# Performance work log

Measured on AMD Instinct MI355X. Metric: run time of the kernel, lower is better.

## Reference

```python
import jax, jax.numpy as jnp
import numpy as np

N_NODES = 100000
N_EDGES = 3200000
N_GRAPHS = 64
F_IN = 64
NUM_CLASSES = 10
CHROM = 21


def _glorot(key, shape):
    fan_in, fan_out = shape
    lim = (6.0 / (fan_in + fan_out)) ** 0.5
    return jax.random.uniform(key, shape, jnp.float32, -lim, lim)


def setup_inputs() -> dict:
    key = jax.random.key(0)
    ks = jax.random.split(key, 16)
    x = jax.random.normal(ks[0], (N_NODES, F_IN), jnp.float32)
    edge_index = jax.random.randint(ks[1], (2, N_EDGES), 0, N_NODES, jnp.int32)
    batch = jnp.sort(jax.random.randint(ks[2], (N_NODES,), 0, N_GRAPHS, jnp.int32))
    return {
        "x": x,
        "edge_index": edge_index,
        "batch": batch,
        # SAGEConv1: 64 -> 16
        "W1l": _glorot(ks[3], (F_IN, 16)), "b1": jnp.zeros((16,), jnp.float32),
        "W1r": _glorot(ks[4], (F_IN, 16)),
        # SAGEConv2: 16 -> 32
        "W2l": _glorot(ks[5], (16, 32)), "b2": jnp.zeros((32,), jnp.float32),
        "W2r": _glorot(ks[6], (16, 32)),
        # SAGEConv3: 32 -> 21
        "W3l": _glorot(ks[7], (32, CHROM)), "b3": jnp.zeros((CHROM,), jnp.float32),
        "W3r": _glorot(ks[8], (32, CHROM)),
        # classifier: 32 -> num_classes
        "Wc": _glorot(ks[9], (32, NUM_CLASSES)), "bc": jnp.zeros((NUM_CLASSES,), jnp.float32),
    }


def _sage_conv(x, src, dst, Wl, b, Wr):
    # mean aggregation of source features at target nodes (PyG SAGEConv default)
    agg = jax.ops.segment_sum(x[src], dst, num_segments=N_NODES)
    cnt = jax.ops.segment_sum(jnp.ones((src.shape[0],), x.dtype), dst, num_segments=N_NODES)
    mean = agg / jnp.maximum(cnt, 1.0)[:, None]
    return mean @ Wl + b + x @ Wr


def reference(x, edge_index, batch, W1l, b1, W1r, W2l, b2, W2r, W3l, b3, W3r, Wc, bc):
    src, dst = edge_index[0], edge_index[1]
    h = jax.nn.relu(_sage_conv(x, src, dst, W1l, b1, W1r))
    h2 = _sage_conv(h, src, dst, W2l, b2, W2r)          # pooled pre-relu
    color = _sage_conv(jax.nn.relu(h2), src, dst, W3l, b3, W3r)
    # global_mean_pool over graphs
    gsum = jax.ops.segment_sum(h2, batch, num_segments=N_GRAPHS)
    gcnt = jax.ops.segment_sum(jnp.ones((h2.shape[0],), h2.dtype), batch, num_segments=N_GRAPHS)
    pooled = gsum / jnp.maximum(gcnt, 1.0)[:, None]
    # dropout p=0.3 is identity in eval mode
    classif = pooled @ Wc + bc
    return classif, color
```

## Files before the change

kernel.cpp:

```cpp
#include <hip/hip_runtime.h>
#include <hip/hip_fp16.h>
#include <cstdint>
#include <cstddef>

#define N_NODES  100000
#define N_EDGES  3200000
#define N_GRAPHS 64

#define BQBITS   9
#define BQ       512
#define NBUCK    196
#define TILE     4096
#define NBLK     782
#define POOL_SLICES 8
#define PADB     4608


__global__ void kp1_hist(const int* __restrict__ dst, int* __restrict__ gh, int ne) {
    __shared__ int h[NBUCK];
    for (int i = threadIdx.x; i < NBUCK; i += 256) h[i] = 0;
    __syncthreads();
    int base = blockIdx.x * TILE;
    for (int i = threadIdx.x; i < TILE; i += 256) {
        int e = base + i;
        if (e < ne) atomicAdd(&h[dst[e] >> BQBITS], 1);
    }
    __syncthreads();
    for (int i = threadIdx.x; i < NBUCK; i += 256) gh[i * NBLK + blockIdx.x] = h[i];
}

__global__ void kp1_scanA(int* __restrict__ gh, int* __restrict__ btotal) {
    int q = blockIdx.x;
    __shared__ int ts[256];
    int v[4];
    int tsum = 0;
#pragma unroll
    for (int u = 0; u < 4; ++u) {
        int idx = threadIdx.x * 4 + u;
        v[u] = (idx < NBLK) ? gh[q * NBLK + idx] : 0;
        tsum += v[u];
    }
    ts[threadIdx.x] = tsum;
    __syncthreads();
    for (int off = 1; off < 256; off <<= 1) {
        int t = (threadIdx.x >= off) ? ts[threadIdx.x - off] : 0;
        __syncthreads();
        ts[threadIdx.x] += t;
        __syncthreads();
    }
    int run = ts[threadIdx.x] - tsum;
#pragma unroll
    for (int u = 0; u < 4; ++u) {
        int idx = threadIdx.x * 4 + u;
        if (idx < NBLK) gh[q * NBLK + idx] = run;
        run += v[u];
    }
    if (threadIdx.x == 255) btotal[q] = ts[255];
}

__global__ void kp1_scanB(const int* __restrict__ btotal, int* __restrict__ bstart) {
    __shared__ int s[256];
    int v = (threadIdx.x < NBUCK) ? btotal[threadIdx.x] : 0;
    s[threadIdx.x] = v;
    __syncthreads();
    for (int off = 1; off < 256; off <<= 1) {
        int t = (threadIdx.x >= off) ? s[threadIdx.x - off] : 0;
        __syncthreads();
        s[threadIdx.x] += t;
        __syncthreads();
    }
    if (threadIdx.x < NBUCK) bstart[threadIdx.x] = s[threadIdx.x] - v;
    if (threadIdx.x == 0) bstart[NBUCK] = N_EDGES;
}

__global__ __launch_bounds__(256) void kp1_scatter(
        const int* __restrict__ src, const int* __restrict__ dst,
        const int* __restrict__ gh, const int* __restrict__ bstart,
        unsigned* __restrict__ tmp, int ne) {
    __shared__ unsigned sed[TILE];
    __shared__ int lcnt[NBUCK];
    __shared__ int lofs[NBUCK + 1];
    __shared__ int fill[NBUCK];
    __shared__ int delta[NBUCK];
    __shared__ int ts[256];
    for (int i = threadIdx.x; i < NBUCK; i += 256) { lcnt[i] = 0; fill[i] = 0; }
    __syncthreads();
    int base = blockIdx.x * TILE;
    int nh = ne - base; if (nh > TILE) nh = TILE;
    int myq[16]; unsigned myw[16];
#pragma unroll
    for (int u = 0; u < 16; ++u) {
        int i = u * 256 + threadIdx.x;
        myq[u] = -1;
        if (i < nh) {
            int d = dst[base + i], s = src[base + i];
            int q = d >> BQBITS;
            myq[u] = q;
            myw[u] = ((unsigned)(d & (BQ - 1)) << 17) | (unsigned)s;
            atomicAdd(&lcnt[q], 1);
        }
    }
    __syncthreads();
    int v = (threadIdx.x < NBUCK) ? lcnt[threadIdx.x] : 0;
    ts[threadIdx.x] = v;
    __syncthreads();
    for (int off = 1; off < 256; off <<= 1) {
        int t = (threadIdx.x >= off) ? ts[threadIdx.x - off] : 0;
        __syncthreads();
        ts[threadIdx.x] += t;
        __syncthreads();
    }
    if (threadIdx.x < NBUCK) {
        int start = ts[threadIdx.x] - v;
        lofs[threadIdx.x] = start;
        delta[threadIdx.x] = bstart[threadIdx.x] + gh[threadIdx.x * NBLK + blockIdx.x] - start;
    }
    if (threadIdx.x == NBUCK - 1) lofs[NBUCK] = ts[threadIdx.x];
    __syncthreads();
#pragma unroll
    for (int u = 0; u < 16; ++u) {
        if (myq[u] >= 0) {
            int r = atomicAdd(&fill[myq[u]], 1);
            sed[lofs[myq[u]] + r] = myw[u];
        }
    }
    __syncthreads();
    for (int p = threadIdx.x; p < nh; p += 256) {
        int lo = 0, hi = NBUCK;
        while (hi - lo > 1) { int mid = (lo + hi) >> 1; if (lofs[mid] <= p) lo = mid; else hi = mid; }
        tmp[p + delta[lo]] = sed[p];
    }
}

__global__ void kp2(const unsigned* __restrict__ tmp, const int* __restrict__ bstart,
                    int* __restrict__ rs, int* __restrict__ deg, int* __restrict__ perm) {
    int q = blockIdx.x;
    int beg = bstart[q], end = bstart[q + 1];
    int m = end - beg;
    int pbase = ((beg + 7) & ~7) + q * PADB;
    __shared__ int cnt[BQ];
    __shared__ int lofs[BQ];
    __shared__ int fill[BQ];
    if (threadIdx.x < BQ) { cnt[threadIdx.x] = 0; fill[threadIdx.x] = 0; }
    __syncthreads();
    for (int p = threadIdx.x; p < m; p += 1024)
        atomicAdd(&cnt[tmp[beg + p] >> 17], 1);
    __syncthreads();
    int pc = 0;
    if (threadIdx.x < BQ) { pc = (cnt[threadIdx.x] + 7) & ~7; lofs[threadIdx.x] = pc; }
    __syncthreads();
    for (int off = 1; off < BQ; off <<= 1) {
        int t = 0;
        if (threadIdx.x < BQ && threadIdx.x >= off) t = lofs[threadIdx.x - off];
        __syncthreads();
        if (threadIdx.x < BQ) lofs[threadIdx.x] += t;
        __syncthreads();
    }
    if (threadIdx.x < BQ) {
        int node = q * BQ + threadIdx.x;
        if (node < N_NODES) {
            int st = lofs[threadIdx.x] - pc;
            rs[node] = pbase + st;
            deg[node] = cnt[threadIdx.x];
            for (int i = cnt[threadIdx.x]; i < pc; ++i)
                perm[pbase + st + i] = N_NODES;
        }
    }
    __syncthreads();
    for (int p = threadIdx.x; p < m; p += 1024) {
        unsigned w = tmp[beg + p];
        int dl = w >> 17;
        int s = w & 0x1FFFF;
        int r = atomicAdd(&fill[dl], 1);
        int st = lofs[dl] - ((cnt[dl] + 7) & ~7);
        perm[pbase + st + r] = s;
    }
}


__global__ void k_zero(__half* __restrict__ y1z, __half* __restrict__ hz,
                       __half* __restrict__ y3z, float* __restrict__ gsum) {
    int t = threadIdx.x;
    if (t < 16) { y1z[t] = __half(0.f); hz[t] = __half(0.f); }
    if (t < 24) y3z[t] = __half(0.f);
    for (int i = t; i < N_GRAPHS * 32; i += 256) gsum[i] = 0.f;
}


__global__ void k_t1(const float* __restrict__ x, const float* __restrict__ W1l,
                     const float* __restrict__ W1r, const float* __restrict__ b1,
                     __half* __restrict__ y1, float* __restrict__ s1, int n) {
    __shared__ float wl[64 * 16], wr[64 * 16], bb[16];
    for (int i = threadIdx.x; i < 64 * 16; i += blockDim.x) { wl[i] = W1l[i]; wr[i] = W1r[i]; }
    if (threadIdx.x < 16) bb[threadIdx.x] = b1[threadIdx.x];
    __syncthreads();
    int node = blockIdx.x * blockDim.x + threadIdx.x;
    if (node >= n) return;
    const float4* xr = reinterpret_cast<const float4*>(x + (size_t)node * 64);
    float accl[16], accr[16];
#pragma unroll
    for (int j = 0; j < 16; ++j) { accl[j] = 0.f; accr[j] = 0.f; }
#pragma unroll
    for (int q = 0; q < 16; ++q) {
        float4 v = xr[q];
        float xs[4] = {v.x, v.y, v.z, v.w};
#pragma unroll
        for (int u = 0; u < 4; ++u) {
            int k = q * 4 + u;
            float xv = xs[u];
#pragma unroll
            for (int j = 0; j < 16; ++j) {
                accl[j] += xv * wl[k * 16 + j];
                accr[j] += xv * wr[k * 16 + j];
            }
        }
    }
    alignas(16) __half yh[16];
#pragma unroll
    for (int j = 0; j < 16; ++j) yh[j] = __float2half(accl[j]);
    uint4* y4 = reinterpret_cast<uint4*>(y1 + (size_t)node * 16);
    const uint4* yv = reinterpret_cast<const uint4*>(yh);
    y4[0] = yv[0]; y4[1] = yv[1];
    float4* s4 = reinterpret_cast<float4*>(s1 + (size_t)node * 16);
#pragma unroll
    for (int q = 0; q < 4; ++q)
        s4[q] = make_float4(accr[q*4+0] + bb[q*4+0], accr[q*4+1] + bb[q*4+1],
                            accr[q*4+2] + bb[q*4+2], accr[q*4+3] + bb[q*4+3]);
}

__global__ void k_t2(const float* __restrict__ mean2, const __half* __restrict__ h,
                     const float* __restrict__ W2l, const float* __restrict__ W2r,
                     const float* __restrict__ b2, float* __restrict__ h2, int n) {
    __shared__ float wl[16 * 32], wr[16 * 32], bb[32];
    for (int i = threadIdx.x; i < 16 * 32; i += blockDim.x) { wl[i] = W2l[i]; wr[i] = W2r[i]; }
    if (threadIdx.x < 32) bb[threadIdx.x] = b2[threadIdx.x];
    __syncthreads();
    int node = blockIdx.x * blockDim.x + threadIdx.x;
    if (node >= n) return;
    float m[16], hh[16];
    const float4* m4 = reinterpret_cast<const float4*>(mean2 + (size_t)node * 16);
#pragma unroll
    for (int q = 0; q < 4; ++q) {
        float4 a = m4[q];
        m[q*4+0]=a.x; m[q*4+1]=a.y; m[q*4+2]=a.z; m[q*4+3]=a.w;
    }
    alignas(16) __half hv[16];
    const uint4* hp = reinterpret_cast<const uint4*>(h + (size_t)node * 16);
    uint4* hvp = reinterpret_cast<uint4*>(hv);
    hvp[0] = hp[0]; hvp[1] = hp[1];
#pragma unroll
    for (int k = 0; k < 16; ++k) hh[k] = __half2float(hv[k]);
    float acc[32];
#pragma unroll
    for (int j = 0; j < 32; ++j) acc[j] = bb[j];
#pragma unroll
    for (int k = 0; k < 16; ++k) {
#pragma unroll
        for (int j = 0; j < 32; ++j)
            acc[j] += m[k] * wl[k * 32 + j] + hh[k] * wr[k * 32 + j];
    }
    float4* o4 = reinterpret_cast<float4*>(h2 + (size_t)node * 32);
#pragma unroll
    for (int q = 0; q < 8; ++q)
        o4[q] = make_float4(acc[q*4+0], acc[q*4+1], acc[q*4+2], acc[q*4+3]);
}

__global__ void k_t3(const float* __restrict__ h2, const float* __restrict__ W3l,
                     const float* __restrict__ W3r, const float* __restrict__ b3,
                     __half* __restrict__ y3, float* __restrict__ s3, int n) {
    __shared__ float wl[32 * 21], wr[32 * 21], bb[21];
    for (int i = threadIdx.x; i < 32 * 21; i += blockDim.x) { wl[i] = W3l[i]; wr[i] = W3r[i]; }
    if (threadIdx.x < 21) bb[threadIdx.x] = b3[threadIdx.x];
    __syncthreads();
    int node = blockIdx.x * blockDim.x + threadIdx.x;
    if (node >= n) return;
    float z[32];
    const float4* h4 = reinterpret_cast<const float4*>(h2 + (size_t)node * 32);
#pragma unroll
    for (int q = 0; q < 8; ++q) {
        float4 v = h4[q];
        z[q*4+0] = fmaxf(v.x, 0.f); z[q*4+1] = fmaxf(v.y, 0.f);
        z[q*4+2] = fmaxf(v.z, 0.f); z[q*4+3] = fmaxf(v.w, 0.f);
    }
    float a[21], c[21];
#pragma unroll
    for (int j = 0; j < 21; ++j) { a[j] = 0.f; c[j] = bb[j]; }
#pragma unroll
    for (int k = 0; k < 32; ++k) {
#pragma unroll
        for (int j = 0; j < 21; ++j) {
            a[j] += z[k] * wl[k * 21 + j];
            c[j] += z[k] * wr[k * 21 + j];
        }
    }
    alignas(16) __half yh[24];
#pragma unroll
    for (int j = 0; j < 21; ++j) yh[j] = __float2half(a[j]);
    yh[21] = __half(0.f); yh[22] = __half(0.f); yh[23] = __half(0.f);
    uint4* yp = reinterpret_cast<uint4*>(y3 + (size_t)node * 24);
    const uint4* yv = reinterpret_cast<const uint4*>(yh);
    yp[0] = yv[0]; yp[1] = yv[1]; yp[2] = yv[2];
    float* so = s3 + (size_t)node * 24;
#pragma unroll
    for (int j = 0; j < 21; ++j) so[j] = c[j];
    so[21] = 0.f; so[22] = 0.f; so[23] = 0.f;
}


__device__ __forceinline__ void acc8(uint4 v, float* a) {
    __half2 h0 = *reinterpret_cast<__half2*>(&v.x);
    __half2 h1 = *reinterpret_cast<__half2*>(&v.y);
    __half2 h2 = *reinterpret_cast<__half2*>(&v.z);
    __half2 h3 = *reinterpret_cast<__half2*>(&v.w);
    float2 f0 = __half22float2(h0), f1 = __half22float2(h1);
    float2 f2 = __half22float2(h2), f3 = __half22float2(h3);
    a[0] += f0.x; a[1] += f0.y; a[2] += f1.x; a[3] += f1.y;
    a[4] += f2.x; a[5] += f2.y; a[6] += f3.x; a[7] += f3.y;
}

template <bool RELU, bool SELF, bool OUT_HALF>
__global__ void k_agg16(const uint4* __restrict__ y, const int* __restrict__ rs,
                        const int* __restrict__ deg, const int* __restrict__ perm,
                        const float* __restrict__ self, void* __restrict__ outp,
                        int n_nodes) {
    int t = blockIdx.x * blockDim.x + threadIdx.x;
    int node = t >> 1;
    int f = t & 1;
    if (node >= n_nodes) return;
    int beg = rs[node];
    int d = deg[node];
    int pend = beg + ((d + 7) & ~7);
    float a[8];
#pragma unroll
    for (int j = 0; j < 8; ++j) a[j] = 0.f;
    for (int e = beg; e < pend; e += 8) {
        const int4* pp = reinterpret_cast<const int4*>(perm + e);
        int4 p0 = pp[0];
        int4 p1 = pp[1];
        uint4 v0 = y[(size_t)p0.x * 2 + f];
        uint4 v1 = y[(size_t)p0.y * 2 + f];
        uint4 v2 = y[(size_t)p0.z * 2 + f];
        uint4 v3 = y[(size_t)p0.w * 2 + f];
        uint4 v4 = y[(size_t)p1.x * 2 + f];
        uint4 v5 = y[(size_t)p1.y * 2 + f];
        uint4 v6 = y[(size_t)p1.z * 2 + f];
        uint4 v7 = y[(size_t)p1.w * 2 + f];
        acc8(v0, a); acc8(v1, a); acc8(v2, a); acc8(v3, a);
        acc8(v4, a); acc8(v5, a); acc8(v6, a); acc8(v7, a);
    }
    float inv = 1.0f / fmaxf((float)d, 1.0f);
#pragma unroll
    for (int j = 0; j < 8; ++j) a[j] *= inv;
    if (SELF) {
        const float4* sp = reinterpret_cast<const float4*>(self + (size_t)node * 16 + f * 8);
        float4 s0 = sp[0], s1 = sp[1];
        a[0] += s0.x; a[1] += s0.y; a[2] += s0.z; a[3] += s0.w;
        a[4] += s1.x; a[5] += s1.y; a[6] += s1.z; a[7] += s1.w;
    }
    if (RELU) {
#pragma unroll
        for (int j = 0; j < 8; ++j) a[j] = fmaxf(a[j], 0.f);
    }
    if constexpr (OUT_HALF) {
        __half2 p0 = __floats2half2_rn(a[0], a[1]);
        __half2 p1 = __floats2half2_rn(a[2], a[3]);
        __half2 p2 = __floats2half2_rn(a[4], a[5]);
        __half2 p3 = __floats2half2_rn(a[6], a[7]);
        uint4 o;
        o.x = *reinterpret_cast<unsigned*>(&p0);
        o.y = *reinterpret_cast<unsigned*>(&p1);
        o.z = *reinterpret_cast<unsigned*>(&p2);
        o.w = *reinterpret_cast<unsigned*>(&p3);
        ((uint4*)outp)[(size_t)node * 2 + f] = o;
    } else {
        float4* op = (float4*)outp + (size_t)node * 4 + f * 2;
        op[0] = make_float4(a[0], a[1], a[2], a[3]);
        op[1] = make_float4(a[4], a[5], a[6], a[7]);
    }
}

__global__ void k_agg21(const uint4* __restrict__ y, const int* __restrict__ rs,
                        const int* __restrict__ deg, const int* __restrict__ perm,
                        const float* __restrict__ self24, float* __restrict__ outp,
                        int n_nodes) {
    int t = blockIdx.x * blockDim.x + threadIdx.x;
    int node = t / 3;
    int f = t - node * 3;
    if (node >= n_nodes) return;
    int beg = rs[node];
    int d = deg[node];
    int pend = beg + ((d + 7) & ~7);
    float a[8];
#pragma unroll
    for (int j = 0; j < 8; ++j) a[j] = 0.f;
    for (int e = beg; e < pend; e += 8) {
        const int4* pp = reinterpret_cast<const int4*>(perm + e);
        int4 p0 = pp[0];
        int4 p1 = pp[1];
        uint4 v0 = y[(size_t)p0.x * 3 + f];
        uint4 v1 = y[(size_t)p0.y * 3 + f];
        uint4 v2 = y[(size_t)p0.z * 3 + f];
        uint4 v3 = y[(size_t)p0.w * 3 + f];
        uint4 v4 = y[(size_t)p1.x * 3 + f];
        uint4 v5 = y[(size_t)p1.y * 3 + f];
        uint4 v6 = y[(size_t)p1.z * 3 + f];
        uint4 v7 = y[(size_t)p1.w * 3 + f];
        acc8(v0, a); acc8(v1, a); acc8(v2, a); acc8(v3, a);
        acc8(v4, a); acc8(v5, a); acc8(v6, a); acc8(v7, a);
    }
    float inv = 1.0f / fmaxf((float)d, 1.0f);
    int c0 = f * 8;
    const float4* sp = reinterpret_cast<const float4*>(self24 + (size_t)node * 24 + c0);
    float4 s0 = sp[0], s1 = sp[1];
    float r[8];
    r[0] = a[0] * inv + s0.x; r[1] = a[1] * inv + s0.y;
    r[2] = a[2] * inv + s0.z; r[3] = a[3] * inv + s0.w;
    r[4] = a[4] * inv + s1.x; r[5] = a[5] * inv + s1.y;
    r[6] = a[6] * inv + s1.z; r[7] = a[7] * inv + s1.w;
    float* op = outp + (size_t)node * 21;
    int nlim = 21 - c0;
#pragma unroll
    for (int j = 0; j < 8; ++j)
        if (j < nlim) op[c0 + j] = r[j];
}


__device__ __forceinline__ int lowerb(const int* a, int n, int key) {
    int lo = 0, hi = n;
    while (lo < hi) { int mid = (lo + hi) >> 1; if (a[mid] < key) lo = mid + 1; else hi = mid; }
    return lo;
}

__global__ void k_pool(const float* __restrict__ h2, const int* __restrict__ batch,
                       float* __restrict__ gsum, float* __restrict__ gcnt, int n) {
    int g = blockIdx.x / POOL_SLICES;
    int slice = blockIdx.x - g * POOL_SLICES;
    __shared__ int sbeg, send;
    if (threadIdx.x == 0) { sbeg = lowerb(batch, n, g); send = lowerb(batch, n, g + 1); }
    __syncthreads();
    int beg = sbeg, end = send;
    int f = threadIdx.x & 31;
    int r = threadIdx.x >> 5;
    float acc = 0.f;
    for (int i = beg + slice * 8 + r; i < end; i += POOL_SLICES * 8)
        acc += h2[(size_t)i * 32 + f];
    __shared__ float red[256];
    red[threadIdx.x] = acc;
    __syncthreads();
    if (r == 0) {
        float s = 0.f;
#pragma unroll
        for (int q = 0; q < 8; ++q) s += red[q * 32 + f];
        atomicAdd(&gsum[g * 32 + f], s);
    }
    if (slice == 0 && threadIdx.x == 0) gcnt[g] = (float)(end - beg);
}

__global__ void k_cls(const float* __restrict__ gsum, const float* __restrict__ gcnt,
                      const float* __restrict__ Wc, const float* __restrict__ bc,
                      float* __restrict__ outp) {
    int t = threadIdx.x;
    if (t >= N_GRAPHS * 10) return;
    int g = t / 10, c = t - g * 10;
    float cv = fmaxf(gcnt[g], 1.f);
    float acc = bc[c];
#pragma unroll
    for (int k = 0; k < 32; ++k) acc += (gsum[g * 32 + k] / cv) * Wc[k * 10 + c];
    outp[g * 10 + c] = acc;
}


extern "C" void kernel_launch(void* const* d_in, const int* in_sizes, int n_in,
                              void* d_out, int out_size, void* d_ws, size_t ws_size,
                              hipStream_t stream) {
    const float* x    = (const float*)d_in[0];
    const int*   ei   = (const int*)d_in[1];
    const int*   batch= (const int*)d_in[2];
    const float* W1l  = (const float*)d_in[3];
    const float* b1   = (const float*)d_in[4];
    const float* W1r  = (const float*)d_in[5];
    const float* W2l  = (const float*)d_in[6];
    const float* b2   = (const float*)d_in[7];
    const float* W2r  = (const float*)d_in[8];
    const float* W3l  = (const float*)d_in[9];
    const float* b3   = (const float*)d_in[10];
    const float* W3r  = (const float*)d_in[11];
    const float* Wc   = (const float*)d_in[12];
    const float* bc   = (const float*)d_in[13];
    float* out = (float*)d_out;

    char* ws = (char*)d_ws;
    size_t off = 0;
    auto alloc = [&](size_t bytes) { size_t o = off; off += (bytes + 255) & ~(size_t)255; return o; };

    int*    rs    = (int*)(ws + alloc((size_t)N_NODES * 4));
    int*    deg   = (int*)(ws + alloc((size_t)N_NODES * 4));
    int*    perm  = (int*)(ws + alloc((size_t)(N_EDGES + (size_t)NBUCK * PADB + 64) * 4));
    int*    gh    = (int*)(ws + alloc((size_t)NBUCK * NBLK * 4));
    int*    btotal= (int*)(ws + alloc(256 * 4));
    int*    bstart= (int*)(ws + alloc(260 * 4));
    __half* y1    = (__half*)(ws + alloc((size_t)(N_NODES + 1) * 16 * 2));
    float*  s1    = (float*)(ws + alloc((size_t)N_NODES * 16 * 4));
    __half* h     = (__half*)(ws + alloc((size_t)(N_NODES + 1) * 16 * 2));
    float*  mean2 = (float*)(ws + alloc((size_t)N_NODES * 16 * 4));
    float*  h2    = (float*)(ws + alloc((size_t)N_NODES * 32 * 4));
    __half* y3    = (__half*)(ws + alloc((size_t)(N_NODES + 1) * 24 * 2));
    float*  s3    = (float*)(ws + alloc((size_t)N_NODES * 24 * 4));
    float*  gsum  = (float*)(ws + alloc((size_t)N_GRAPHS * 32 * 4));
    float*  gcnt  = (float*)(ws + alloc((size_t)N_GRAPHS * 4));

    unsigned* tmp = (unsigned*)h2;

    const int* src = ei;
    const int* dst = ei + N_EDGES;

    int nb  = (N_NODES + 255) / 256;
    int g2  = (N_NODES * 2 + 255) / 256;
    int g3  = (N_NODES * 3 + 255) / 256;

    k_zero<<<1, 256, 0, stream>>>(y1 + (size_t)N_NODES * 16, h + (size_t)N_NODES * 16,
                                  y3 + (size_t)N_NODES * 24, gsum);

    kp1_hist   <<<NBLK, 256, 0, stream>>>(dst, gh, N_EDGES);
    kp1_scanA  <<<NBUCK, 256, 0, stream>>>(gh, btotal);
    kp1_scanB  <<<1, 256, 0, stream>>>(btotal, bstart);
    kp1_scatter<<<NBLK, 256, 0, stream>>>(src, dst, gh, bstart, tmp, N_EDGES);
    kp2        <<<NBUCK, 1024, 0, stream>>>(tmp, bstart, rs, deg, perm);

    k_t1<<<nb, 256, 0, stream>>>(x, W1l, W1r, b1, y1, s1, N_NODES);
    k_agg16<true, true, true><<<g2, 256, 0, stream>>>(
        (const uint4*)y1, rs, deg, perm, s1, h, N_NODES);

    k_agg16<false, false, false><<<g2, 256, 0, stream>>>(
        (const uint4*)h, rs, deg, perm, nullptr, mean2, N_NODES);
    k_t2<<<nb, 256, 0, stream>>>(mean2, h, W2l, W2r, b2, h2, N_NODES);

    k_t3<<<nb, 256, 0, stream>>>(h2, W3l, W3r, b3, y3, s3, N_NODES);
    k_agg21<<<g3, 256, 0, stream>>>(
        (const uint4*)y3, rs, deg, perm, s3, out + N_GRAPHS * 10, N_NODES);

    k_pool<<<N_GRAPHS * POOL_SLICES, 256, 0, stream>>>(h2, batch, gsum, gcnt, N_NODES);
    k_cls<<<1, 640, 0, stream>>>(gsum, gcnt, Wc, bc, out);
}
```

Before: 237.8 us.

## Store gathered node features in FP8 e4m3 to halve gather traffic

```diff
diff --git a/kernel.cpp b/kernel.cpp
--- a/kernel.cpp
+++ b/kernel.cpp
@@ -1,5 +1,6 @@
 #include <hip/hip_runtime.h>
 #include <hip/hip_fp16.h>
+#include <hip/hip_fp8.h>
 #include <cstdint>
 #include <cstddef>
 
@@ -178,18 +179,41 @@
 }
 
 
-__global__ void k_zero(__half* __restrict__ y1z, __half* __restrict__ hz,
-                       __half* __restrict__ y3z, float* __restrict__ gsum) {
+__device__ __forceinline__ void accq(uint2 v, float* a) {
+    unsigned x = v.x, y = v.y;
+#pragma unroll
+    for (int j = 0; j < 4; ++j) {
+        __hip_fp8_e4m3 q0, q1;
+        q0.__x = (__hip_fp8_storage_t)((x >> (8 * j)) & 0xFF);
+        q1.__x = (__hip_fp8_storage_t)((y >> (8 * j)) & 0xFF);
+        a[j]     += (float)q0;
+        a[4 + j] += (float)q1;
+    }
+}
+
+__device__ __forceinline__ uint2 pack8_fp8(const float* a) {
+    unsigned lo = 0, hi = 0;
+#pragma unroll
+    for (int j = 0; j < 4; ++j) {
+        lo |= (unsigned)__hip_fp8_e4m3(a[j]).__x << (8 * j);
+        hi |= (unsigned)__hip_fp8_e4m3(a[4 + j]).__x << (8 * j);
+    }
+    uint2 o; o.x = lo; o.y = hi; return o;
+}
+
+
+__global__ void k_zero(uint2* __restrict__ y1qz, uint2* __restrict__ hqz,
+                       unsigned char* __restrict__ y3qz, float* __restrict__ gsum) {
     int t = threadIdx.x;
-    if (t < 16) { y1z[t] = __half(0.f); hz[t] = __half(0.f); }
-    if (t < 24) y3z[t] = __half(0.f);
+    if (t < 2) { y1qz[t] = make_uint2(0, 0); hqz[t] = make_uint2(0, 0); }
+    if (t < 24) y3qz[t] = 0;
     for (int i = t; i < N_GRAPHS * 32; i += 256) gsum[i] = 0.f;
 }
 
 
 __global__ void k_t1(const float* __restrict__ x, const float* __restrict__ W1l,
                      const float* __restrict__ W1r, const float* __restrict__ b1,
-                     __half* __restrict__ y1, float* __restrict__ s1, int n) {
+                     uint2* __restrict__ y1q, float* __restrict__ s1, int n) {
     __shared__ float wl[64 * 16], wr[64 * 16], bb[16];
     for (int i = threadIdx.x; i < 64 * 16; i += blockDim.x) { wl[i] = W1l[i]; wr[i] = W1r[i]; }
     if (threadIdx.x < 16) bb[threadIdx.x] = b1[threadIdx.x];
@@ -215,12 +239,8 @@
             }
         }
     }
-    alignas(16) __half yh[16];
-#pragma unroll
-    for (int j = 0; j < 16; ++j) yh[j] = __float2half(accl[j]);
-    uint4* y4 = reinterpret_cast<uint4*>(y1 + (size_t)node * 16);
-    const uint4* yv = reinterpret_cast<const uint4*>(yh);
-    y4[0] = yv[0]; y4[1] = yv[1];
+    y1q[(size_t)node * 2 + 0] = pack8_fp8(accl);
+    y1q[(size_t)node * 2 + 1] = pack8_fp8(accl + 8);
     float4* s4 = reinterpret_cast<float4*>(s1 + (size_t)node * 16);
 #pragma unroll
     for (int q = 0; q < 4; ++q)
@@ -267,7 +287,7 @@
 
 __global__ void k_t3(const float* __restrict__ h2, const float* __restrict__ W3l,
                      const float* __restrict__ W3r, const float* __restrict__ b3,
-                     __half* __restrict__ y3, float* __restrict__ s3, int n) {
+                     unsigned char* __restrict__ y3q, float* __restrict__ s3, int n) {
     __shared__ float wl[32 * 21], wr[32 * 21], bb[21];
     for (int i = threadIdx.x; i < 32 * 21; i += blockDim.x) { wl[i] = W3l[i]; wr[i] = W3r[i]; }
     if (threadIdx.x < 21) bb[threadIdx.x] = b3[threadIdx.x];
@@ -282,9 +302,10 @@
         z[q*4+0] = fmaxf(v.x, 0.f); z[q*4+1] = fmaxf(v.y, 0.f);
         z[q*4+2] = fmaxf(v.z, 0.f); z[q*4+3] = fmaxf(v.w, 0.f);
     }
-    float a[21], c[21];
+    float a[24], c[21];
 #pragma unroll
     for (int j = 0; j < 21; ++j) { a[j] = 0.f; c[j] = bb[j]; }
+    a[21] = 0.f; a[22] = 0.f; a[23] = 0.f;
 #pragma unroll
     for (int k = 0; k < 32; ++k) {
 #pragma unroll
@@ -293,13 +314,10 @@
             c[j] += z[k] * wr[k * 21 + j];
         }
     }
-    alignas(16) __half yh[24];
-#pragma unroll
-    for (int j = 0; j < 21; ++j) yh[j] = __float2half(a[j]);
-    yh[21] = __half(0.f); yh[22] = __half(0.f); yh[23] = __half(0.f);
-    uint4* yp = reinterpret_cast<uint4*>(y3 + (size_t)node * 24);
-    const uint4* yv = reinterpret_cast<const uint4*>(yh);
-    yp[0] = yv[0]; yp[1] = yv[1]; yp[2] = yv[2];
+    uint2* yp = reinterpret_cast<uint2*>(y3q + (size_t)node * 24);
+    yp[0] = pack8_fp8(a);
+    yp[1] = pack8_fp8(a + 8);
+    yp[2] = pack8_fp8(a + 16);
     float* so = s3 + (size_t)node * 24;
 #pragma unroll
     for (int j = 0; j < 21; ++j) so[j] = c[j];
@@ -307,22 +325,10 @@
 }
 
 
-__device__ __forceinline__ void acc8(uint4 v, float* a) {
-    __half2 h0 = *reinterpret_cast<__half2*>(&v.x);
-    __half2 h1 = *reinterpret_cast<__half2*>(&v.y);
-    __half2 h2 = *reinterpret_cast<__half2*>(&v.z);
-    __half2 h3 = *reinterpret_cast<__half2*>(&v.w);
-    float2 f0 = __half22float2(h0), f1 = __half22float2(h1);
-    float2 f2 = __half22float2(h2), f3 = __half22float2(h3);
-    a[0] += f0.x; a[1] += f0.y; a[2] += f1.x; a[3] += f1.y;
-    a[4] += f2.x; a[5] += f2.y; a[6] += f3.x; a[7] += f3.y;
-}
-
-template <bool RELU, bool SELF, bool OUT_HALF>
-__global__ void k_agg16(const uint4* __restrict__ y, const int* __restrict__ rs,
-                        const int* __restrict__ deg, const int* __restrict__ perm,
-                        const float* __restrict__ self, void* __restrict__ outp,
-                        int n_nodes) {
+__global__ void k_agg_l1(const uint2* __restrict__ yq, const int* __restrict__ rs,
+                         const int* __restrict__ deg, const int* __restrict__ perm,
+                         const float* __restrict__ s1, __half* __restrict__ h,
+                         uint2* __restrict__ hq, int n_nodes) {
     int t = blockIdx.x * blockDim.x + threadIdx.x;
     int node = t >> 1;
     int f = t & 1;
@@ -337,55 +343,47 @@
         const int4* pp = reinterpret_cast<const int4*>(perm + e);
         int4 p0 = pp[0];
         int4 p1 = pp[1];
-        uint4 v0 = y[(size_t)p0.x * 2 + f];
-        uint4 v1 = y[(size_t)p0.y * 2 + f];
-        uint4 v2 = y[(size_t)p0.z * 2 + f];
-        uint4 v3 = y[(size_t)p0.w * 2 + f];
-        uint4 v4 = y[(size_t)p1.x * 2 + f];
-        uint4 v5 = y[(size_t)p1.y * 2 + f];
-        uint4 v6 = y[(size_t)p1.z * 2 + f];
-        uint4 v7 = y[(size_t)p1.w * 2 + f];
-        acc8(v0, a); acc8(v1, a); acc8(v2, a); acc8(v3, a);
-        acc8(v4, a); acc8(v5, a); acc8(v6, a); acc8(v7, a);
+        uint2 v0 = yq[(size_t)p0.x * 2 + f];
+        uint2 v1 = yq[(size_t)p0.y * 2 + f];
+        uint2 v2 = yq[(size_t)p0.z * 2 + f];
+        uint2 v3 = yq[(size_t)p0.w * 2 + f];
+        uint2 v4 = yq[(size_t)p1.x * 2 + f];
+        uint2 v5 = yq[(size_t)p1.y * 2 + f];
+        uint2 v6 = yq[(size_t)p1.z * 2 + f];
+        uint2 v7 = yq[(size_t)p1.w * 2 + f];
+        accq(v0, a); accq(v1, a); accq(v2, a); accq(v3, a);
+        accq(v4, a); accq(v5, a); accq(v6, a); accq(v7, a);
     }
     float inv = 1.0f / fmaxf((float)d, 1.0f);
-#pragma unroll
-    for (int j = 0; j < 8; ++j) a[j] *= inv;
-    if (SELF) {
-        const float4* sp = reinterpret_cast<const float4*>(self + (size_t)node * 16 + f * 8);
-        float4 s0 = sp[0], s1 = sp[1];
-        a[0] += s0.x; a[1] += s0.y; a[2] += s0.z; a[3] += s0.w;
-        a[4] += s1.x; a[5] += s1.y; a[6] += s1.z; a[7] += s1.w;
-    }
-    if (RELU) {
-#pragma unroll
-        for (int j = 0; j < 8; ++j) a[j] = fmaxf(a[j], 0.f);
-    }
-    if constexpr (OUT_HALF) {
-        __half2 p0 = __floats2half2_rn(a[0], a[1]);
-        __half2 p1 = __floats2half2_rn(a[2], a[3]);
-        __half2 p2 = __floats2half2_rn(a[4], a[5]);
-        __half2 p3 = __floats2half2_rn(a[6], a[7]);
-        uint4 o;
-        o.x = *reinterpret_cast<unsigned*>(&p0);
-        o.y = *reinterpret_cast<unsigned*>(&p1);
-        o.z = *reinterpret_cast<unsigned*>(&p2);
-        o.w = *reinterpret_cast<unsigned*>(&p3);
-        ((uint4*)outp)[(size_t)node * 2 + f] = o;
-    } else {
-        float4* op = (float4*)outp + (size_t)node * 4 + f * 2;
-        op[0] = make_float4(a[0], a[1], a[2], a[3]);
-        op[1] = make_float4(a[4], a[5], a[6], a[7]);
-    }
-}
-
-__global__ void k_agg21(const uint4* __restrict__ y, const int* __restrict__ rs,
-                        const int* __restrict__ deg, const int* __restrict__ perm,
-                        const float* __restrict__ self24, float* __restrict__ outp,
-                        int n_nodes) {
+    const float4* sp = reinterpret_cast<const float4*>(s1 + (size_t)node * 16 + f * 8);
+    float4 s0 = sp[0], s1v = sp[1];
+    a[0] = fmaxf(a[0] * inv + s0.x, 0.f);
+    a[1] = fmaxf(a[1] * inv + s0.y, 0.f);
+    a[2] = fmaxf(a[2] * inv + s0.z, 0.f);
+    a[3] = fmaxf(a[3] * inv + s0.w, 0.f);
+    a[4] = fmaxf(a[4] * inv + s1v.x, 0.f);
+    a[5] = fmaxf(a[5] * inv + s1v.y, 0.f);
+    a[6] = fmaxf(a[6] * inv + s1v.z, 0.f);
+    a[7] = fmaxf(a[7] * inv + s1v.w, 0.f);
+    __half2 p0h = __floats2half2_rn(a[0], a[1]);
+    __half2 p1h = __floats2half2_rn(a[2], a[3]);
+    __half2 p2h = __floats2half2_rn(a[4], a[5]);
+    __half2 p3h = __floats2half2_rn(a[6], a[7]);
+    uint4 o;
+    o.x = *reinterpret_cast<unsigned*>(&p0h);
+    o.y = *reinterpret_cast<unsigned*>(&p1h);
+    o.z = *reinterpret_cast<unsigned*>(&p2h);
+    o.w = *reinterpret_cast<unsigned*>(&p3h);
+    reinterpret_cast<uint4*>(h)[(size_t)node * 2 + f] = o;
+    hq[(size_t)node * 2 + f] = pack8_fp8(a);
+}
+
+__global__ void k_agg_l2(const uint2* __restrict__ hq, const int* __restrict__ rs,
+                         const int* __restrict__ deg, const int* __restrict__ perm,
+                         float* __restrict__ mean2, int n_nodes) {
     int t = blockIdx.x * blockDim.x + threadIdx.x;
-    int node = t / 3;
-    int f = t - node * 3;
+    int node = t >> 1;
+    int f = t & 1;
     if (node >= n_nodes) return;
     int beg = rs[node];
     int d = deg[node];
@@ -397,16 +395,52 @@
         const int4* pp = reinterpret_cast<const int4*>(perm + e);
         int4 p0 = pp[0];
         int4 p1 = pp[1];
-        uint4 v0 = y[(size_t)p0.x * 3 + f];
-        uint4 v1 = y[(size_t)p0.y * 3 + f];
-        uint4 v2 = y[(size_t)p0.z * 3 + f];
-        uint4 v3 = y[(size_t)p0.w * 3 + f];
-        uint4 v4 = y[(size_t)p1.x * 3 + f];
-        uint4 v5 = y[(size_t)p1.y * 3 + f];
-        uint4 v6 = y[(size_t)p1.z * 3 + f];
-        uint4 v7 = y[(size_t)p1.w * 3 + f];
-        acc8(v0, a); acc8(v1, a); acc8(v2, a); acc8(v3, a);
-        acc8(v4, a); acc8(v5, a); acc8(v6, a); acc8(v7, a);
+        uint2 v0 = hq[(size_t)p0.x * 2 + f];
+        uint2 v1 = hq[(size_t)p0.y * 2 + f];
+        uint2 v2 = hq[(size_t)p0.z * 2 + f];
+        uint2 v3 = hq[(size_t)p0.w * 2 + f];
+        uint2 v4 = hq[(size_t)p1.x * 2 + f];
+        uint2 v5 = hq[(size_t)p1.y * 2 + f];
+        uint2 v6 = hq[(size_t)p1.z * 2 + f];
+        uint2 v7 = hq[(size_t)p1.w * 2 + f];
+        accq(v0, a); accq(v1, a); accq(v2, a); accq(v3, a);
+        accq(v4, a); accq(v5, a); accq(v6, a); accq(v7, a);
+    }
+    float inv = 1.0f / fmaxf((float)d, 1.0f);
+    float4* op = reinterpret_cast<float4*>(mean2 + (size_t)node * 16 + f * 8);
+    op[0] = make_float4(a[0] * inv, a[1] * inv, a[2] * inv, a[3] * inv);
+    op[1] = make_float4(a[4] * inv, a[5] * inv, a[6] * inv, a[7] * inv);
+}
+
+__global__ void k_agg_l3(const unsigned char* __restrict__ y3q, const int* __restrict__ rs,
+                         const int* __restrict__ deg, const int* __restrict__ perm,
+                         const float* __restrict__ self24, float* __restrict__ outp,
+                         int n_nodes) {
+    int t = blockIdx.x * blockDim.x + threadIdx.x;
+    int node = t / 3;
+    int f = t - node * 3;
+    if (node >= n_nodes) return;
+    const uint2* yq = reinterpret_cast<const uint2*>(y3q);
+    int beg = rs[node];
+    int d = deg[node];
+    int pend = beg + ((d + 7) & ~7);
+    float a[8];
+#pragma unroll
+    for (int j = 0; j < 8; ++j) a[j] = 0.f;
+    for (int e = beg; e < pend; e += 8) {
+        const int4* pp = reinterpret_cast<const int4*>(perm + e);
+        int4 p0 = pp[0];
+        int4 p1 = pp[1];
+        uint2 v0 = yq[(size_t)p0.x * 3 + f];
+        uint2 v1 = yq[(size_t)p0.y * 3 + f];
+        uint2 v2 = yq[(size_t)p0.z * 3 + f];
+        uint2 v3 = yq[(size_t)p0.w * 3 + f];
+        uint2 v4 = yq[(size_t)p1.x * 3 + f];
+        uint2 v5 = yq[(size_t)p1.y * 3 + f];
+        uint2 v6 = yq[(size_t)p1.z * 3 + f];
+        uint2 v7 = yq[(size_t)p1.w * 3 + f];
+        accq(v0, a); accq(v1, a); accq(v2, a); accq(v3, a);
+        accq(v4, a); accq(v5, a); accq(v6, a); accq(v7, a);
     }
     float inv = 1.0f / fmaxf((float)d, 1.0f);
     int c0 = f * 8;
@@ -499,12 +533,13 @@
     int*    gh    = (int*)(ws + alloc((size_t)NBUCK * NBLK * 4));
     int*    btotal= (int*)(ws + alloc(256 * 4));
     int*    bstart= (int*)(ws + alloc(260 * 4));
-    __half* y1    = (__half*)(ws + alloc((size_t)(N_NODES + 1) * 16 * 2));
+    uint2*  y1q   = (uint2*)(ws + alloc((size_t)(N_NODES + 1) * 16));
     float*  s1    = (float*)(ws + alloc((size_t)N_NODES * 16 * 4));
-    __half* h     = (__half*)(ws + alloc((size_t)(N_NODES + 1) * 16 * 2));
+    __half* h     = (__half*)(ws + alloc((size_t)N_NODES * 16 * 2));
+    uint2*  hq    = (uint2*)(ws + alloc((size_t)(N_NODES + 1) * 16));
     float*  mean2 = (float*)(ws + alloc((size_t)N_NODES * 16 * 4));
     float*  h2    = (float*)(ws + alloc((size_t)N_NODES * 32 * 4));
-    __half* y3    = (__half*)(ws + alloc((size_t)(N_NODES + 1) * 24 * 2));
+    unsigned char* y3q = (unsigned char*)(ws + alloc((size_t)(N_NODES + 1) * 24));
     float*  s3    = (float*)(ws + alloc((size_t)N_NODES * 24 * 4));
     float*  gsum  = (float*)(ws + alloc((size_t)N_GRAPHS * 32 * 4));
     float*  gcnt  = (float*)(ws + alloc((size_t)N_GRAPHS * 4));
@@ -518,8 +553,8 @@
     int g2  = (N_NODES * 2 + 255) / 256;
     int g3  = (N_NODES * 3 + 255) / 256;
 
-    k_zero<<<1, 256, 0, stream>>>(y1 + (size_t)N_NODES * 16, h + (size_t)N_NODES * 16,
-                                  y3 + (size_t)N_NODES * 24, gsum);
+    k_zero<<<1, 256, 0, stream>>>(y1q + (size_t)N_NODES * 2, hq + (size_t)N_NODES * 2,
+                                  y3q + (size_t)N_NODES * 24, gsum);
 
     kp1_hist   <<<NBLK, 256, 0, stream>>>(dst, gh, N_EDGES);
     kp1_scanA  <<<NBUCK, 256, 0, stream>>>(gh, btotal);
@@ -527,17 +562,14 @@
     kp1_scatter<<<NBLK, 256, 0, stream>>>(src, dst, gh, bstart, tmp, N_EDGES);
     kp2        <<<NBUCK, 1024, 0, stream>>>(tmp, bstart, rs, deg, perm);
 
-    k_t1<<<nb, 256, 0, stream>>>(x, W1l, W1r, b1, y1, s1, N_NODES);
-    k_agg16<true, true, true><<<g2, 256, 0, stream>>>(
-        (const uint4*)y1, rs, deg, perm, s1, h, N_NODES);
-
-    k_agg16<false, false, false><<<g2, 256, 0, stream>>>(
-        (const uint4*)h, rs, deg, perm, nullptr, mean2, N_NODES);
+    k_t1<<<nb, 256, 0, stream>>>(x, W1l, W1r, b1, y1q, s1, N_NODES);
+    k_agg_l1<<<g2, 256, 0, stream>>>(y1q, rs, deg, perm, s1, h, hq, N_NODES);
+
+    k_agg_l2<<<g2, 256, 0, stream>>>(hq, rs, deg, perm, mean2, N_NODES);
     k_t2<<<nb, 256, 0, stream>>>(mean2, h, W2l, W2r, b2, h2, N_NODES);
 
-    k_t3<<<nb, 256, 0, stream>>>(h2, W3l, W3r, b3, y3, s3, N_NODES);
-    k_agg21<<<g3, 256, 0, stream>>>(
-        (const uint4*)y3, rs, deg, perm, s3, out + N_GRAPHS * 10, N_NODES);
+    k_t3<<<nb, 256, 0, stream>>>(h2, W3l, W3r, b3, y3q, s3, N_NODES);
+    k_agg_l3<<<g3, 256, 0, stream>>>(y3q, rs, deg, perm, s3, out + N_GRAPHS * 10, N_NODES);
 
     k_pool<<<N_GRAPHS * POOL_SLICES, 256, 0, stream>>>(h2, batch, gsum, gcnt, N_NODES);
     k_cls<<<1, 640, 0, stream>>>(gsum, gcnt, Wc, bc, out);
```

Result: slower. 293.3 us (+23.3%).
